# Performance work log

Measured on AMD Instinct MI355X. Metric: run time of the kernel, lower is better.

The kernel has to match this reference:

```python
import jax, jax.numpy as jnp
import numpy as np
import math

B, S, D = 4, 2048, 1024
H = 1
HD = D // H  # head_dim == hidden_dim since num_heads=1 (required by source's phase_encoder Linear)
HALF = HD // 2
SYNC_LOSS_WEIGHT = 0.01


def setup_inputs() -> dict:
    key = jax.random.key(0)
    ks = jax.random.split(key, 11)
    wstd = 0.02
    inp = {
        "x": jax.random.normal(ks[0], (B, S, D), dtype=jnp.float32),
        "Wq": jax.random.normal(ks[1], (D, D), dtype=jnp.float32) * wstd,
        "bq": jnp.zeros((D,), jnp.float32),
        "Wk": jax.random.normal(ks[2], (D, D), dtype=jnp.float32) * wstd,
        "bk": jnp.zeros((D,), jnp.float32),
        "Wv": jax.random.normal(ks[3], (D, D), dtype=jnp.float32) * wstd,
        "bv": jnp.zeros((D,), jnp.float32),
        "Wp": jax.random.normal(ks[4], (D, D), dtype=jnp.float32) * wstd,
        "bp": jnp.zeros((D,), jnp.float32),
        "Wo": jax.random.normal(ks[5], (D, D), dtype=jnp.float32) * wstd,
        "bo": jnp.zeros((D,), jnp.float32),
        "bifurcation_param": jnp.asarray(1.0, jnp.float32),
        "phase_coupling": jnp.asarray(0.5, jnp.float32),
    }
    return inp


def _phase(t, Wp, bp):
    # t: [B,H,S,HD] -> instantaneous phase via angle(complex(first_half, second_half))
    pf = t @ Wp.T + bp
    re, im = pf[..., :HALF], pf[..., HALF:]
    return jnp.arctan2(im, re)  # [B,H,S,HALF]


def reference(x, Wq, bq, Wk, bk, Wv, bv, Wp, bp, Wo, bo, bifurcation_param, phase_coupling):
    b, s, d = x.shape
    Q = (x @ Wq.T + bq).reshape(b, s, H, HD).transpose(0, 2, 1, 3)  # [B,H,S,HD]
    K = (x @ Wk.T + bk).reshape(b, s, H, HD).transpose(0, 2, 1, 3)
    V = (x @ Wv.T + bv).reshape(b, s, H, HD).transpose(0, 2, 1, 3)

    scores = jnp.einsum("bhqd,bhkd->bhqk", Q, K) / math.sqrt(HD)

    pQ = _phase(Q, Wp, bp)
    pK = _phase(K, Wp, bp)
    # mean_d cos(pQ - pK) == (cos(pQ)@cos(pK)^T + sin(pQ)@sin(pK)^T) / HALF
    sync = (jnp.einsum("bhqd,bhkd->bhqk", jnp.cos(pQ), jnp.cos(pK))
            + jnp.einsum("bhqd,bhkd->bhqk", jnp.sin(pQ), jnp.sin(pK))) / HALF

    t = jnp.tanh(scores)
    bif = bifurcation_param * t * (1.0 - t)

    chaotic = scores + phase_coupling * sync + bif
    attn = jax.nn.softmax(chaotic, axis=-1)

    av = jnp.einsum("bhqk,bhkd->bhqd", attn, V)
    av = av.transpose(0, 2, 1, 3).reshape(b, s, d)
    out = av @ Wo.T + bo

    # torch.var default: unbiased (ddof=1), over last dim of sync
    sync_loss = SYNC_LOSS_WEIGHT * jnp.var(sync, axis=-1, ddof=1).mean()
    return out, sync_loss
```

## Files before the change

kernel.cpp:

```cpp
#include <hip/hip_runtime.h>
#include <hip/hip_bf16.h>
#include <math.h>

#define S_LEN 2048
#define D_MODEL 1024
#define N_BATCH 4
#define N_HALF 512

typedef unsigned short u16;
typedef __attribute__((ext_vector_type(8))) short bf16x8;
typedef __attribute__((ext_vector_type(4))) float f32x4;

__device__ inline u16 f2bf(float v) {
  __hip_bfloat16 h = __float2bfloat16(v);
  return *reinterpret_cast<u16*>(&h);
}
__device__ inline float bf2f(u16 u) {
  __hip_bfloat16 h = *reinterpret_cast<__hip_bfloat16*>(&u);
  return __bfloat162float(h);
}
__device__ inline void gl2lds16(const void* g, void* l) {
  __builtin_amdgcn_global_load_lds(
      (const __attribute__((address_space(1))) unsigned int*)g,
      (__attribute__((address_space(3))) unsigned int*)l, 16, 0, 0);
// ... 58 lines not shown
    float v = t[c][r0 + r];
    long long idx = (long long)(bx + r0 + r) * D_MODEL + by + c;
    u16 h = f2bf(v);
    hi[idx] = h;
    lo[idx] = f2bf(v - bf2f(h));
  }
}
__global__ __launch_bounds__(256)
void w2_bias(const float* __restrict__ Wo, const float* __restrict__ bv,
             float* __restrict__ w2b) {
  const int d = blockIdx.x;
  const int tid = threadIdx.x;
  float acc = 0.f;
  for (int j = tid; j < D_MODEL; j += 256)
    acc += Wo[(long long)d * D_MODEL + j] * bv[j];
#pragma unroll
  for (int m = 1; m < 64; m <<= 1) acc += __shfl_xor(acc, m);
  __shared__ float red[4];
  if ((tid & 63) == 0) red[tid >> 6] = acc;
  __syncthreads();
  if (tid == 0) w2b[d] = red[0] + red[1] + red[2] + red[3];
}


__global__ __launch_bounds__(256, 2)
void qk_fused(const u16* __restrict__ X, const u16* __restrict__ Wq,
              const u16* __restrict__ Wk,
              const float* __restrict__ bq, const float* __restrict__ bk,
              u16* __restrict__ Qo, u16* __restrict__ Ko) {
  __shared__ u16 Xs[128 * 64];
  __shared__ u16 Qs[128 * 64];
  __shared__ u16 Ks[128 * 64];
  const int tid  = threadIdx.x;
  const int wave = tid >> 6;
  const int lane = tid & 63;
  const int quad = lane >> 4;
  const int tc   = lane & 15;
  const int bm = blockIdx.y * 128;
  const int bn = blockIdx.x * 128;
  const int wm = (wave & 1) * 64;
  const int wn = (wave >> 1) * 64;

  f32x4 acc1[4][4], acc2[4][4];
#pragma unroll
  for (int i = 0; i < 4; i++)
#pragma unroll
    for (int j = 0; j < 4; j++) {
      acc1[i][j] = (f32x4){0.f, 0.f, 0.f, 0.f};
      acc2[i][j] = (f32x4){0.f, 0.f, 0.f, 0.f};
    }

  const int srow8 = lane >> 3;
  const int scol  = ((lane & 7) ^ srow8) * 8;
  const int srowb = wave * 32;
  const u16* gx = X  + (long long)(bm + srowb + srow8) * D_MODEL + scol;
  const u16* gq = Wq + (long long)(bn + srowb + srow8) * D_MODEL + scol;
  const u16* gk = Wk + (long long)(bn + srowb + srow8) * D_MODEL + scol;
  const int wb = srowb * 64;
  const long long r8 = 8LL * D_MODEL;
  const int swzA = tc & 7;

  for (int k0 = 0; k0 < D_MODEL; k0 += 64) {
#pragma unroll
    for (int c = 0; c < 4; c++) {
      gl2lds16(gx + c * r8, Xs + wb + c * 512);
      gl2lds16(gq + c * r8, Qs + wb + c * 512);
      gl2lds16(gk + c * r8, Ks + wb + c * 512);
    }
    gx += 64; gq += 64; gk += 64;
    __syncthreads();
    bf16x8 af[4][2], bq4[4][2], bk4[4][2];
#pragma unroll
    for (int i = 0; i < 4; i++) {
      const int ra = (wm + i * 16 + tc) * 64;
      const int rb = (wn + i * 16 + tc) * 64;
#pragma unroll
      for (int ks = 0; ks < 2; ks++) {
        const int co = ((ks * 4 + quad) ^ swzA) * 8;
        af[i][ks]  = *(const bf16x8*)(Xs + ra + co);
        bq4[i][ks] = *(const bf16x8*)(Qs + rb + co);
        bk4[i][ks] = *(const bf16x8*)(Ks + rb + co);
      }
    }
#pragma unroll
    for (int i = 0; i < 4; i++)
#pragma unroll
      for (int j = 0; j < 4; j++) {
        acc1[i][j] = __builtin_amdgcn_mfma_f32_16x16x32_bf16(af[i][0], bq4[j][0], acc1[i][j], 0, 0, 0);
        acc2[i][j] = __builtin_amdgcn_mfma_f32_16x16x32_bf16(af[i][0], bk4[j][0], acc2[i][j], 0, 0, 0);
        acc1[i][j] = __builtin_amdgcn_mfma_f32_16x16x32_bf16(af[i][1], bq4[j][1], acc1[i][j], 0, 0, 0);
        acc2[i][j] = __builtin_amdgcn_mfma_f32_16x16x32_bf16(af[i][1], bk4[j][1], acc2[i][j], 0, 0, 0);
      }
    __syncthreads();
  }

#pragma unroll
  for (int i = 0; i < 4; i++) {
    const int row0 = bm + wm + i * 16 + quad * 4;
#pragma unroll
    for (int j = 0; j < 4; j++) {
      const int col = bn + wn + j * 16 + tc;
#pragma unroll
      for (int r = 0; r < 4; r++) {
        long long idx = (long long)(row0 + r) * D_MODEL + col;
        Qo[idx] = f2bf(acc1[i][j][r] + bq[col]);
        Ko[idx] = f2bf(acc2[i][j][r] + bk[col]);
      }
    }
  }
}

__global__ __launch_bounds__(256, 2)
void pf_fused(const u16* __restrict__ Qb, const u16* __restrict__ Wp,
              const float* __restrict__ bp,
              u16* __restrict__ pfQ, u16* __restrict__ pfK,
              long long TDo) {
  __shared__ u16 lds_all[3 * 128 * 64];
  u16* Qs = lds_all;
  u16* Ks = lds_all + 128 * 64;
  u16* Ws = lds_all + 2 * 128 * 64;
  const int tid  = threadIdx.x;
  const int wave = tid >> 6;
  const int lane = tid & 63;
  const int quad = lane >> 4;
  const int tc   = lane & 15;
  const int bm = blockIdx.y * 128;
  const int bn = blockIdx.x * 64;
  const int wm = (wave & 1) * 64;
  const int grp = wave >> 1;
// ... 75 lines not shown
#pragma unroll
      for (int i = 2 * half; i < 2 * half + 2; i++)
#pragma unroll
        for (int j = 0; j < 4; j++) {
          f32x4 own = *(const f32x4*)(ex + wave * 2048 + cnt * 256 + lane * 4);
          f32x4 oth = *(const f32x4*)(ex + (wave ^ 2) * 2048 + cnt * 256 + lane * 4);
          const int row0 = bm + wm + i * 16 + quad * 4;
          const long long col = colbase + j * 16 + tc;
#pragma unroll
          for (int r = 0; r < 4; r++) {
            float a = own[r], p = oth[r];
            float n2 = a * a + p * p;
            float outv = (grp == 0) ? 1.f : 0.f;
            if (n2 > 0.f) outv = a * (1.0f / sqrtf(n2));
            Ou[(long long)(row0 + r) * D_MODEL + col] = f2bf(outv);
          }
          cnt++;
        }
      __syncthreads();
    }
  }
}

__global__ __launch_bounds__(256)
void mfma_gemm_out3(const u16* __restrict__ Ah, const u16* __restrict__ Al,
                    const u16* __restrict__ Bh, const u16* __restrict__ Bl,
                    const float* __restrict__ bias, float* __restrict__ C,
                    int N, int K) {
  __shared__ u16 Ash[128 * 64];
  __shared__ u16 Asl[128 * 64];
  __shared__ u16 Bsh[128 * 64];
  __shared__ u16 Bsl[128 * 64];
  const int tid  = threadIdx.x;
  const int wave = tid >> 6;
  const int lane = tid & 63;
  const int quad = lane >> 4;
  const int tc   = lane & 15;
  const int bm = blockIdx.y * 128;
  const int bn = blockIdx.x * 128;
  const int wm = (wave & 1) * 64;
  const int wn = (wave >> 1) * 64;

  f32x4 acc[4][4];
#pragma unroll
  for (int i = 0; i < 4; i++)
#pragma unroll
    for (int j = 0; j < 4; j++) acc[i][j] = (f32x4){0.f, 0.f, 0.f, 0.f};

  const int srow8 = lane >> 3;
  const int scol  = ((lane & 7) ^ srow8) * 8;
  const int srowb = wave * 32;
  long long aoff = (long long)(bm + srowb + srow8) * K + scol;
  long long boff = (long long)(bn + srowb + srow8) * K + scol;
  const u16 *gah = Ah + aoff, *gal = Al + aoff;
  const u16 *gbh = Bh + boff, *gbl = Bl + boff;
  const int wb = srowb * 64;
  const long long r8K = 8LL * K;
  const int swzA = tc & 7;

  for (int k0 = 0; k0 < K; k0 += 64) {
#pragma unroll
    for (int c = 0; c < 4; c++) {
      gl2lds16(gah + c * r8K, Ash + wb + c * 512);
      gl2lds16(gal + c * r8K, Asl + wb + c * 512);
      gl2lds16(gbh + c * r8K, Bsh + wb + c * 512);
      gl2lds16(gbl + c * r8K, Bsl + wb + c * 512);
    }
    gah += 64; gal += 64; gbh += 64; gbl += 64;
    __syncthreads();
    bf16x8 ah[4][2], al[4][2], bh[4][2], bl[4][2];
#pragma unroll
    for (int i = 0; i < 4; i++) {
      const int ra = (wm + i * 16 + tc) * 64;
      const int rb = (wn + i * 16 + tc) * 64;
#pragma unroll
      for (int ks = 0; ks < 2; ks++) {
        const int co = ((ks * 4 + quad) ^ swzA) * 8;
        ah[i][ks] = *(const bf16x8*)(Ash + ra + co);
        al[i][ks] = *(const bf16x8*)(Asl + ra + co);
        bh[i][ks] = *(const bf16x8*)(Bsh + rb + co);
        bl[i][ks] = *(const bf16x8*)(Bsl + rb + co);
      }
    }
#pragma unroll
    for (int i = 0; i < 4; i++)
#pragma unroll
      for (int j = 0; j < 4; j++) {
#pragma unroll
        for (int ks = 0; ks < 2; ks++) {
          acc[i][j] = __builtin_amdgcn_mfma_f32_16x16x32_bf16(ah[i][ks], bh[j][ks], acc[i][j], 0, 0, 0);
          acc[i][j] = __builtin_amdgcn_mfma_f32_16x16x32_bf16(ah[i][ks], bl[j][ks], acc[i][j], 0, 0, 0);
          acc[i][j] = __builtin_amdgcn_mfma_f32_16x16x32_bf16(al[i][ks], bh[j][ks], acc[i][j], 0, 0, 0);
        }
      }
    __syncthreads();
  }
#pragma unroll
  for (int i = 0; i < 4; i++) {
    const int row0 = bm + wm + i * 16 + quad * 4;
#pragma unroll
    for (int j = 0; j < 4; j++) {
      const int col = bn + wn + j * 16 + tc;
      float b = bias ? bias[col] : 0.f;
#pragma unroll
      for (int r = 0; r < 4; r++)
        C[(long long)(row0 + r) * N + col] = acc[i][j][r] + b;
    }
  }
}

__global__ __launch_bounds__(256)
void vwt_kernel(const u16* __restrict__ W2h, const u16* __restrict__ W2l,
                const u16* __restrict__ X, const float* __restrict__ w2b,
                u16* __restrict__ Ch, u16* __restrict__ Cl,
                long long sB, long long sC) {
  __shared__ u16 Ah[128 * 64];
  __shared__ u16 Al[128 * 64];
  __shared__ u16 Bs[128 * 64];
  const int tid  = threadIdx.x;
  const int wave = tid >> 6;
  const int lane = tid & 63;
  const int quad = lane >> 4;
  const int tc   = lane & 15;
  const int bm = blockIdx.y * 128;
  const int bn = blockIdx.x * 128;
  const long long z = blockIdx.z;
  const int wm = (wave & 1) * 64;
  const int wn = (wave >> 1) * 64;

  f32x4 acc[4][4];
#pragma unroll
  for (int i = 0; i < 4; i++)
#pragma unroll
    for (int j = 0; j < 4; j++) acc[i][j] = (f32x4){0.f, 0.f, 0.f, 0.f};

  const int srow8 = lane >> 3;
  const int scol  = ((lane & 7) ^ srow8) * 8;
  const int srowb = wave * 32;
  const long long aoff = (long long)(bm + srowb + srow8) * D_MODEL + scol;
  const u16* gah = W2h + aoff;
  const u16* gal = W2l + aoff;
  const u16* gb  = X + z * sB + (long long)(bn + srowb + srow8) * D_MODEL + scol;
  const int wb = srowb * 64;
  const long long r8 = 8LL * D_MODEL;
  const int swzA = tc & 7;

  for (int k0 = 0; k0 < D_MODEL; k0 += 64) {
#pragma unroll
    for (int c = 0; c < 4; c++) {
      gl2lds16(gah + c * r8, Ah + wb + c * 512);
      gl2lds16(gal + c * r8, Al + wb + c * 512);
      gl2lds16(gb  + c * r8, Bs + wb + c * 512);
    }
    gah += 64; gal += 64; gb += 64;
    __syncthreads();
    bf16x8 ah4[4][2], al4[4][2], bx[4][2];
#pragma unroll
    for (int i = 0; i < 4; i++) {
      const int ra = (wm + i * 16 + tc) * 64;
      const int rb = (wn + i * 16 + tc) * 64;
#pragma unroll
      for (int ks = 0; ks < 2; ks++) {
        const int co = ((ks * 4 + quad) ^ swzA) * 8;
        ah4[i][ks] = *(const bf16x8*)(Ah + ra + co);
        al4[i][ks] = *(const bf16x8*)(Al + ra + co);
        bx[i][ks]  = *(const bf16x8*)(Bs + rb + co);
      }
    }
#pragma unroll
    for (int i = 0; i < 4; i++)
#pragma unroll
      for (int j = 0; j < 4; j++) {
        acc[i][j] = __builtin_amdgcn_mfma_f32_16x16x32_bf16(ah4[i][0], bx[j][0], acc[i][j], 0, 0, 0);
        acc[i][j] = __builtin_amdgcn_mfma_f32_16x16x32_bf16(al4[i][0], bx[j][0], acc[i][j], 0, 0, 0);
        acc[i][j] = __builtin_amdgcn_mfma_f32_16x16x32_bf16(ah4[i][1], bx[j][1], acc[i][j], 0, 0, 0);
        acc[i][j] = __builtin_amdgcn_mfma_f32_16x16x32_bf16(al4[i][1], bx[j][1], acc[i][j], 0, 0, 0);
      }
    __syncthreads();
  }

  u16* Chz = Ch + z * sC;
  u16* Clz = Cl + z * sC;
#pragma unroll
  for (int i = 0; i < 4; i++) {
    const int row0 = bm + wm + i * 16 + quad * 4;
#pragma unroll
    for (int j = 0; j < 4; j++) {
      const int col = bn + wn + j * 16 + tc;
#pragma unroll
      for (int r = 0; r < 4; r++) {
        float v = acc[i][j][r] + w2b[row0 + r];
        long long idx = (long long)(row0 + r) * S_LEN + col;
        u16 h = f2bf(v);
        Chz[idx] = h;
        Clz[idx] = f2bf(v - bf2f(h));
      }
    }
  }
}

__global__ __launch_bounds__(256)
void gemm_bsplit(const u16* __restrict__ A,
                 const u16* __restrict__ Bh, const u16* __restrict__ Bl,
                 const float* __restrict__ bias, float* __restrict__ C,
                 int N, int K, long long sA, long long sB, long long sC) {
  __shared__ u16 As[128 * 64];
  __shared__ u16 Bsh[128 * 64];
  __shared__ u16 Bsl[128 * 64];
  const int tid  = threadIdx.x;
  const int wave = tid >> 6;
  const int lane = tid & 63;
  const int quad = lane >> 4;
  const int tc   = lane & 15;
  const int bm = blockIdx.y * 128;
  const int bn = blockIdx.x * 128;
  const long long z = blockIdx.z;
  const int wm = (wave & 1) * 64;
  const int wn = (wave >> 1) * 64;
// ... 40 lines not shown
#pragma unroll
    for (int i = 0; i < 4; i++)
#pragma unroll
      for (int j = 0; j < 4; j++) {
        acc[i][j] = __builtin_amdgcn_mfma_f32_16x16x32_bf16(af[i][0], bh[j][0], acc[i][j], 0, 0, 0);
        acc[i][j] = __builtin_amdgcn_mfma_f32_16x16x32_bf16(af[i][0], bl[j][0], acc[i][j], 0, 0, 0);
        acc[i][j] = __builtin_amdgcn_mfma_f32_16x16x32_bf16(af[i][1], bh[j][1], acc[i][j], 0, 0, 0);
        acc[i][j] = __builtin_amdgcn_mfma_f32_16x16x32_bf16(af[i][1], bl[j][1], acc[i][j], 0, 0, 0);
      }
    __syncthreads();
  }

  float* Cz = C + z * sC;
#pragma unroll
  for (int i = 0; i < 4; i++) {
    const int row0 = bm + wm + i * 16 + quad * 4;
#pragma unroll
    for (int j = 0; j < 4; j++) {
      const int col = bn + wn + j * 16 + tc;
#pragma unroll
      for (int r = 0; r < 4; r++)
        Cz[(long long)(row0 + r) * N + col] = acc[i][j][r] + bias[col];
    }
  }
}

__global__ __launch_bounds__(256, 2)
void chaotic_fused(const u16* __restrict__ Q, const u16* __restrict__ Kt,
                   const u16* __restrict__ Uq, const u16* __restrict__ Uk,
                   float* __restrict__ Cc,
                   float* __restrict__ ssum, float* __restrict__ ssq,
                   const float* __restrict__ bifp, const float* __restrict__ pcp) {
  __shared__ u16 Qs[128 * 64];
  __shared__ u16 Ks[128 * 64];
  __shared__ u16 Us[128 * 64];
  __shared__ u16 Ws[128 * 64];
  const int tid  = threadIdx.x;
  const int wave = tid >> 6;
  const int lane = tid & 63;
  const int quad = lane >> 4;
  const int tc   = lane & 15;
  const int bm = blockIdx.y * 128;
  const int bn = blockIdx.x * 128;
  const long long z = blockIdx.z;
  const long long sQ = (long long)S_LEN * D_MODEL;
  const int wm = (wave & 1) * 64;
  const int wn = (wave >> 1) * 64;

  f32x4 acc1[4][4], acc2[4][4];
#pragma unroll
  for (int i = 0; i < 4; i++)
#pragma unroll
    for (int j = 0; j < 4; j++) {
      acc1[i][j] = (f32x4){0.f, 0.f, 0.f, 0.f};
      acc2[i][j] = (f32x4){0.f, 0.f, 0.f, 0.f};
    }

  const int srow8  = lane >> 3;
  const int scol   = ((lane & 7) ^ srow8) * 8;
  const int srowb  = wave * 32;
  const u16* gq = Q  + z * sQ + (long long)(bm + srowb + srow8) * D_MODEL + scol;
  const u16* gk = Kt + z * sQ + (long long)(bn + srowb + srow8) * D_MODEL + scol;
  const u16* gu = Uq + z * sQ + (long long)(bm + srowb + srow8) * D_MODEL + scol;
  const u16* gw = Uk + z * sQ + (long long)(bn + srowb + srow8) * D_MODEL + scol;
  const int wb = srowb * 64;
  const long long r8 = 8LL * D_MODEL;

  const int swzA = tc & 7;

  for (int k0 = 0; k0 < D_MODEL; k0 += 64) {
#pragma unroll
    for (int c = 0; c < 4; c++) {
      gl2lds16(gq + c * r8, Qs + wb + c * 512);
      gl2lds16(gk + c * r8, Ks + wb + c * 512);
      gl2lds16(gu + c * r8, Us + wb + c * 512);
      gl2lds16(gw + c * r8, Ws + wb + c * 512);
    }
    gq += 64; gk += 64; gu += 64; gw += 64;
    __syncthreads();
    {
      bf16x8 af[4][2], bg[4][2];
#pragma unroll
      for (int i = 0; i < 4; i++) {
        const int ra = (wm + i * 16 + tc) * 64;
        const int rb = (wn + i * 16 + tc) * 64;
#pragma unroll
        for (int ks = 0; ks < 2; ks++) {
          const int co = ((ks * 4 + quad) ^ swzA) * 8;
          af[i][ks] = *(const bf16x8*)(Qs + ra + co);
          bg[i][ks] = *(const bf16x8*)(Ks + rb + co);
        }
      }
#pragma unroll
      for (int i = 0; i < 4; i++)
#pragma unroll
        for (int j = 0; j < 4; j++) {
          acc1[i][j] = __builtin_amdgcn_mfma_f32_16x16x32_bf16(af[i][0], bg[j][0], acc1[i][j], 0, 0, 0);
          acc1[i][j] = __builtin_amdgcn_mfma_f32_16x16x32_bf16(af[i][1], bg[j][1], acc1[i][j], 0, 0, 0);
        }
    }
    {
      bf16x8 cf[4][2], dg[4][2];
#pragma unroll
      for (int i = 0; i < 4; i++) {
        const int ra = (wm + i * 16 + tc) * 64;
        const int rb = (wn + i * 16 + tc) * 64;
#pragma unroll
        for (int ks = 0; ks < 2; ks++) {
          const int co = ((ks * 4 + quad) ^ swzA) * 8;
          cf[i][ks] = *(const bf16x8*)(Us + ra + co);
          dg[i][ks] = *(const bf16x8*)(Ws + rb + co);
        }
      }
#pragma unroll
      for (int i = 0; i < 4; i++)
#pragma unroll
        for (int j = 0; j < 4; j++) {
          acc2[i][j] = __builtin_amdgcn_mfma_f32_16x16x32_bf16(cf[i][0], dg[j][0], acc2[i][j], 0, 0, 0);
          acc2[i][j] = __builtin_amdgcn_mfma_f32_16x16x32_bf16(cf[i][1], dg[j][1], acc2[i][j], 0, 0, 0);
        }
    }
    __syncthreads();
  }

  const float bif = *bifp;
  const float pc  = *pcp;
  float rsum[4][4], rsq[4][4];
#pragma unroll
  for (int i = 0; i < 4; i++)
#pragma unroll
    for (int r = 0; r < 4; r++) { rsum[i][r] = 0.f; rsq[i][r] = 0.f; }

  float* C = Cc + z * (long long)S_LEN * S_LEN;
#pragma unroll
  for (int i = 0; i < 4; i++) {
    const int row0 = bm + wm + i * 16 + quad * 4;
#pragma unroll
    for (int j = 0; j < 4; j++) {
      const int col = bn + wn + j * 16 + tc;
#pragma unroll
      for (int r = 0; r < 4; r++) {
        float sc = acc1[i][j][r] * 0.03125f;
        float sy = acc2[i][j][r] * (1.0f / 512.0f);
        float t  = fast_tanh(sc);
        C[(long long)(row0 + r) * S_LEN + col] = sc + pc * sy + bif * t * (1.0f - t);
        rsum[i][r] += sy;
        rsq[i][r]  += sy * sy;
      }
    }
  }
#pragma unroll
  for (int m = 1; m < 16; m <<= 1) {
#pragma unroll
    for (int i = 0; i < 4; i++)
#pragma unroll
      for (int r = 0; r < 4; r++) {
        rsum[i][r] += __shfl_xor(rsum[i][r], m);
        rsq[i][r]  += __shfl_xor(rsq[i][r], m);
      }
  }
  if (tc == 0) {
#pragma unroll
    for (int i = 0; i < 4; i++)
#pragma unroll
      for (int r = 0; r < 4; r++) {
        long long rr = z * S_LEN + bm + wm + i * 16 + quad * 4 + r;
        atomicAdd(&ssum[rr], rsum[i][r]);
        atomicAdd(&ssq[rr],  rsq[i][r]);
      }
  }
}

__global__ __launch_bounds__(256)
void softmax_bf(const float* __restrict__ Cc, u16* __restrict__ P) {
  const long long row = (long long)blockIdx.y * S_LEN + blockIdx.x;
  const int tid = threadIdx.x;
  const float* p = Cc + row * S_LEN + tid * 8;
  u16* q = P + row * S_LEN + tid * 8;
  float4 a = *(const float4*)p;
  float4 b = *(const float4*)(p + 4);
  float v[8] = {a.x, a.y, a.z, a.w, b.x, b.y, b.z, b.w};
  float m = v[0];
#pragma unroll
  for (int i = 1; i < 8; i++) m = fmaxf(m, v[i]);
#pragma unroll
  for (int mask = 1; mask < 64; mask <<= 1) m = fmaxf(m, __shfl_xor(m, mask));
  __shared__ float red[8];
  if ((tid & 63) == 0) red[tid >> 6] = m;
  __syncthreads();
  m = fmaxf(fmaxf(red[0], red[1]), fmaxf(red[2], red[3]));
  float s = 0.f;
#pragma unroll
// ... 60 lines not shown

  u16* xbf   = (u16*)d_ws;
  u16* wqb   = xbf + TD;
  u16* wkb   = wqb + WSZ;
  u16* wpb   = wkb + WSZ;
  u16* woh   = wpb + WSZ;
  u16* wol   = woh + WSZ;
  u16* wvth  = wol + WSZ;
  u16* wvtl  = wvth + WSZ;
  u16* w2h   = wvtl + WSZ;
  u16* w2l   = w2h + WSZ;
  float* W2f = (float*)(w2l + WSZ);
  float* w2b = W2f + WSZ;
  u16* Qbf   = (u16*)(w2b + D_MODEL);
  u16* Kbf   = Qbf + TD;
  u16* pfQ   = Kbf + TD;
  u16* pfK   = pfQ + TD;
  float* Cc  = (float*)(pfK + TD);
  float* ssum = Cc + (long long)N_BATCH * S_LEN * S_LEN;
  float* ssq  = ssum + NROW;
  u16* attn = Qbf;
  u16* vwh  = pfQ;
  u16* vwl  = pfK;

  dim3 blk(256);
  const long long sQ = (long long)S_LEN * D_MODEL;
  const long long sS = (long long)S_LEN * S_LEN;

  cast_bf4_multi<<<11264, blk, 0, stream>>>(x, xbf, Wq, wqb, Wk, wkb, Wp, wpb);
  cast_split<<<(int)(WSZ / 4 / 256), blk, 0, stream>>>(Wo, woh, wol, WSZ / 4);
  transpose_split<<<dim3(32, 32), blk, 0, stream>>>(Wv, wvth, wvtl);
  mfma_gemm_out3<<<dim3(8, 8, 1), blk, 0, stream>>>(
      woh, wol, wvth, wvtl, nullptr, W2f, D_MODEL, D_MODEL);
  cast_split<<<(int)(WSZ / 4 / 256), blk, 0, stream>>>(W2f, w2h, w2l, WSZ / 4);
  w2_bias<<<D_MODEL, blk, 0, stream>>>(Wo, bv, w2b);

  qk_fused<<<dim3(8, 64), blk, 0, stream>>>(xbf, wqb, wkb, bq, bk, Qbf, Kbf);
  pf_fused<<<dim3(8, 64), blk, 0, stream>>>(Qbf, wpb, bp, pfQ, pfK, TD);
  hipMemsetAsync(ssum, 0, (size_t)(2 * NROW) * sizeof(float), stream);

  chaotic_fused<<<dim3(16, 16, N_BATCH), blk, 0, stream>>>(
      Qbf, Kbf, pfQ, pfK, Cc, ssum, ssq, bifp, pcp);
  vwt_kernel<<<dim3(16, 8, N_BATCH), blk, 0, stream>>>(
      w2h, w2l, xbf, w2b, vwh, vwl, sQ, sQ);
  softmax_bf<<<dim3(S_LEN, N_BATCH), blk, 0, stream>>>(Cc, attn);
  gemm_bsplit<<<dim3(8, 16, N_BATCH), blk, 0, stream>>>(
      attn, vwh, vwl, bo, out,
      D_MODEL, S_LEN, sS, sQ, sQ);
  syncloss_kernel<<<1, 1024, 0, stream>>>(ssum, ssq, out + TD);
}
```

Before: 484.1 us.

## Merge independent GEMM launches into combined heterogeneous-block kernels

Merges the W2 = Wo·Wv split-precision GEMM into the QK projection kernel as extra blocks, and merges the chaotic score kernel with the V·W2 transform kernel into one launch with interleaved block roles. The aim is to fill the GPU better with independent work in the same launch and to cut launch gaps. The V·W2 output goes to a separate workspace buffer when space allows, because the original location aliases pfQ/pfK, which the chaotic blocks read concurrently. Otherwise it falls back to two sequential launches. The cost is more LDS per block in the merged kernels, plus possible imbalance between block types.

```diff
diff --git a/kernel.cpp b/kernel.cpp
--- a/kernel.cpp
+++ b/kernel.cpp
@@ -104,89 +104,164 @@
   if (tid == 0) w2b[d] = red[0] + red[1] + red[2] + red[3];
 }
 
-
 __global__ __launch_bounds__(256, 2)
-void qk_fused(const u16* __restrict__ X, const u16* __restrict__ Wq,
-              const u16* __restrict__ Wk,
-              const float* __restrict__ bq, const float* __restrict__ bk,
-              u16* __restrict__ Qo, u16* __restrict__ Ko) {
-  __shared__ u16 Xs[128 * 64];
-  __shared__ u16 Qs[128 * 64];
-  __shared__ u16 Ks[128 * 64];
+void qk_out3(const u16* __restrict__ X, const u16* __restrict__ Wq,
+             const u16* __restrict__ Wk,
+             const float* __restrict__ bq, const float* __restrict__ bk,
+             u16* __restrict__ Qo, u16* __restrict__ Ko,
+             const u16* __restrict__ Ah3, const u16* __restrict__ Al3,
+             const u16* __restrict__ Bh3, const u16* __restrict__ Bl3,
+             float* __restrict__ W2f) {
+  __shared__ __align__(16) u16 smem[4 * 128 * 64];
+  const int id   = blockIdx.x;
   const int tid  = threadIdx.x;
   const int wave = tid >> 6;
   const int lane = tid & 63;
   const int quad = lane >> 4;
   const int tc   = lane & 15;
-  const int bm = blockIdx.y * 128;
-  const int bn = blockIdx.x * 128;
   const int wm = (wave & 1) * 64;
   const int wn = (wave >> 1) * 64;
-
-  f32x4 acc1[4][4], acc2[4][4];
-#pragma unroll
-  for (int i = 0; i < 4; i++)
-#pragma unroll
-    for (int j = 0; j < 4; j++) {
-      acc1[i][j] = (f32x4){0.f, 0.f, 0.f, 0.f};
-      acc2[i][j] = (f32x4){0.f, 0.f, 0.f, 0.f};
-    }
-
   const int srow8 = lane >> 3;
   const int scol  = ((lane & 7) ^ srow8) * 8;
   const int srowb = wave * 32;
-  const u16* gx = X  + (long long)(bm + srowb + srow8) * D_MODEL + scol;
-  const u16* gq = Wq + (long long)(bn + srowb + srow8) * D_MODEL + scol;
-  const u16* gk = Wk + (long long)(bn + srowb + srow8) * D_MODEL + scol;
   const int wb = srowb * 64;
   const long long r8 = 8LL * D_MODEL;
   const int swzA = tc & 7;
 
-  for (int k0 = 0; k0 < D_MODEL; k0 += 64) {
-#pragma unroll
-    for (int c = 0; c < 4; c++) {
-      gl2lds16(gx + c * r8, Xs + wb + c * 512);
-      gl2lds16(gq + c * r8, Qs + wb + c * 512);
-      gl2lds16(gk + c * r8, Ks + wb + c * 512);
-    }
-    gx += 64; gq += 64; gk += 64;
-    __syncthreads();
-    bf16x8 af[4][2], bq4[4][2], bk4[4][2];
+  if (id < 64) {
+    u16* Ash = smem;
+    u16* Asl = smem + 8192;
+    u16* Bsh = smem + 16384;
+    u16* Bsl = smem + 24576;
+    const int bm = (id >> 3) * 128;
+    const int bn = (id & 7) * 128;
+
+    f32x4 acc[4][4];
+#pragma unroll
+    for (int i = 0; i < 4; i++)
+#pragma unroll
+      for (int j = 0; j < 4; j++) acc[i][j] = (f32x4){0.f, 0.f, 0.f, 0.f};
+
+    long long aoff = (long long)(bm + srowb + srow8) * D_MODEL + scol;
+    long long boff = (long long)(bn + srowb + srow8) * D_MODEL + scol;
+    const u16 *gah = Ah3 + aoff, *gal = Al3 + aoff;
+    const u16 *gbh = Bh3 + boff, *gbl = Bl3 + boff;
+
+    for (int k0 = 0; k0 < D_MODEL; k0 += 64) {
+#pragma unroll
+      for (int c = 0; c < 4; c++) {
+        gl2lds16(gah + c * r8, Ash + wb + c * 512);
+        gl2lds16(gal + c * r8, Asl + wb + c * 512);
+        gl2lds16(gbh + c * r8, Bsh + wb + c * 512);
+        gl2lds16(gbl + c * r8, Bsl + wb + c * 512);
+      }
+      gah += 64; gal += 64; gbh += 64; gbl += 64;
+      __syncthreads();
+      bf16x8 ah[4][2], al[4][2], bh[4][2], bl[4][2];
+#pragma unroll
+      for (int i = 0; i < 4; i++) {
+        const int ra = (wm + i * 16 + tc) * 64;
+        const int rb = (wn + i * 16 + tc) * 64;
+#pragma unroll
+        for (int ks = 0; ks < 2; ks++) {
+          const int co = ((ks * 4 + quad) ^ swzA) * 8;
+          ah[i][ks] = *(const bf16x8*)(Ash + ra + co);
+          al[i][ks] = *(const bf16x8*)(Asl + ra + co);
+          bh[i][ks] = *(const bf16x8*)(Bsh + rb + co);
+          bl[i][ks] = *(const bf16x8*)(Bsl + rb + co);
+        }
+      }
+#pragma unroll
+      for (int i = 0; i < 4; i++)
+#pragma unroll
+        for (int j = 0; j < 4; j++) {
+#pragma unroll
+          for (int ks = 0; ks < 2; ks++) {
+            acc[i][j] = __builtin_amdgcn_mfma_f32_16x16x32_bf16(ah[i][ks], bh[j][ks], acc[i][j], 0, 0, 0);
+            acc[i][j] = __builtin_amdgcn_mfma_f32_16x16x32_bf16(ah[i][ks], bl[j][ks], acc[i][j], 0, 0, 0);
+            acc[i][j] = __builtin_amdgcn_mfma_f32_16x16x32_bf16(al[i][ks], bh[j][ks], acc[i][j], 0, 0, 0);
+          }
+        }
+      __syncthreads();
+    }
 #pragma unroll
     for (int i = 0; i < 4; i++) {
-      const int ra = (wm + i * 16 + tc) * 64;
-      const int rb = (wn + i * 16 + tc) * 64;
-#pragma unroll
-      for (int ks = 0; ks < 2; ks++) {
-        const int co = ((ks * 4 + quad) ^ swzA) * 8;
-        af[i][ks]  = *(const bf16x8*)(Xs + ra + co);
-        bq4[i][ks] = *(const bf16x8*)(Qs + rb + co);
-        bk4[i][ks] = *(const bf16x8*)(Ks + rb + co);
-      }
-    }
+      const int row0 = bm + wm + i * 16 + quad * 4;
+#pragma unroll
+      for (int j = 0; j < 4; j++) {
+        const int col = bn + wn + j * 16 + tc;
+#pragma unroll
+        for (int r = 0; r < 4; r++)
+          W2f[(long long)(row0 + r) * D_MODEL + col] = acc[i][j][r];
+      }
+    }
+  } else {
+    u16* Xs = smem;
+    u16* Qs = smem + 8192;
+    u16* Ks = smem + 16384;
+    const int qid = id - 64;
+    const int bn = (qid & 7) * 128;
+    const int bm = (qid >> 3) * 128;
+
+    f32x4 acc1[4][4], acc2[4][4];
 #pragma unroll
     for (int i = 0; i < 4; i++)
 #pragma unroll
       for (int j = 0; j < 4; j++) {
-        acc1[i][j] = __builtin_amdgcn_mfma_f32_16x16x32_bf16(af[i][0], bq4[j][0], acc1[i][j], 0, 0, 0);
-        acc2[i][j] = __builtin_amdgcn_mfma_f32_16x16x32_bf16(af[i][0], bk4[j][0], acc2[i][j], 0, 0, 0);
-        acc1[i][j] = __builtin_amdgcn_mfma_f32_16x16x32_bf16(af[i][1], bq4[j][1], acc1[i][j], 0, 0, 0);
-        acc2[i][j] = __builtin_amdgcn_mfma_f32_16x16x32_bf16(af[i][1], bk4[j][1], acc2[i][j], 0, 0, 0);
-      }
-    __syncthreads();
-  }
-
-#pragma unroll
-  for (int i = 0; i < 4; i++) {
-    const int row0 = bm + wm + i * 16 + quad * 4;
-#pragma unroll
-    for (int j = 0; j < 4; j++) {
-      const int col = bn + wn + j * 16 + tc;
-#pragma unroll
-      for (int r = 0; r < 4; r++) {
-        long long idx = (long long)(row0 + r) * D_MODEL + col;
-        Qo[idx] = f2bf(acc1[i][j][r] + bq[col]);
-        Ko[idx] = f2bf(acc2[i][j][r] + bk[col]);
+        acc1[i][j] = (f32x4){0.f, 0.f, 0.f, 0.f};
+        acc2[i][j] = (f32x4){0.f, 0.f, 0.f, 0.f};
+      }
+
+    const u16* gx = X  + (long long)(bm + srowb + srow8) * D_MODEL + scol;
+    const u16* gq = Wq + (long long)(bn + srowb + srow8) * D_MODEL + scol;
+    const u16* gk = Wk + (long long)(bn + srowb + srow8) * D_MODEL + scol;
+
+    for (int k0 = 0; k0 < D_MODEL; k0 += 64) {
+#pragma unroll
+      for (int c = 0; c < 4; c++) {
+        gl2lds16(gx + c * r8, Xs + wb + c * 512);
+        gl2lds16(gq + c * r8, Qs + wb + c * 512);
+        gl2lds16(gk + c * r8, Ks + wb + c * 512);
+      }
+      gx += 64; gq += 64; gk += 64;
+      __syncthreads();
+      bf16x8 af[4][2], bq4[4][2], bk4[4][2];
+#pragma unroll
+      for (int i = 0; i < 4; i++) {
+        const int ra = (wm + i * 16 + tc) * 64;
+        const int rb = (wn + i * 16 + tc) * 64;
+#pragma unroll
+        for (int ks = 0; ks < 2; ks++) {
+          const int co = ((ks * 4 + quad) ^ swzA) * 8;
+          af[i][ks]  = *(const bf16x8*)(Xs + ra + co);
+          bq4[i][ks] = *(const bf16x8*)(Qs + rb + co);
+          bk4[i][ks] = *(const bf16x8*)(Ks + rb + co);
+        }
+      }
+#pragma unroll
+      for (int i = 0; i < 4; i++)
+#pragma unroll
+        for (int j = 0; j < 4; j++) {
+          acc1[i][j] = __builtin_amdgcn_mfma_f32_16x16x32_bf16(af[i][0], bq4[j][0], acc1[i][j], 0, 0, 0);
+          acc2[i][j] = __builtin_amdgcn_mfma_f32_16x16x32_bf16(af[i][0], bk4[j][0], acc2[i][j], 0, 0, 0);
+          acc1[i][j] = __builtin_amdgcn_mfma_f32_16x16x32_bf16(af[i][1], bq4[j][1], acc1[i][j], 0, 0, 0);
+          acc2[i][j] = __builtin_amdgcn_mfma_f32_16x16x32_bf16(af[i][1], bk4[j][1], acc2[i][j], 0, 0, 0);
+        }
+      __syncthreads();
+    }
+
+#pragma unroll
+    for (int i = 0; i < 4; i++) {
+      const int row0 = bm + wm + i * 16 + quad * 4;
+#pragma unroll
+      for (int j = 0; j < 4; j++) {
+        const int col = bn + wn + j * 16 + tc;
+#pragma unroll
+        for (int r = 0; r < 4; r++) {
+          long long idx = (long long)(row0 + r) * D_MODEL + col;
+          Qo[idx] = f2bf(acc1[i][j][r] + bq[col]);
+          Ko[idx] = f2bf(acc2[i][j][r] + bk[col]);
+        }
       }
     }
   }
@@ -308,178 +383,235 @@
   }
 }
 
-__global__ __launch_bounds__(256)
-void mfma_gemm_out3(const u16* __restrict__ Ah, const u16* __restrict__ Al,
-                    const u16* __restrict__ Bh, const u16* __restrict__ Bl,
-                    const float* __restrict__ bias, float* __restrict__ C,
-                    int N, int K) {
-  __shared__ u16 Ash[128 * 64];
-  __shared__ u16 Asl[128 * 64];
-  __shared__ u16 Bsh[128 * 64];
-  __shared__ u16 Bsl[128 * 64];
+__global__ __launch_bounds__(256, 2)
+void chaotic_vwt(const u16* __restrict__ Q, const u16* __restrict__ Kt,
+                 const u16* __restrict__ Uq, const u16* __restrict__ Uk,
+                 float* __restrict__ Cc,
+                 float* __restrict__ ssum, float* __restrict__ ssq,
+                 const float* __restrict__ bifp, const float* __restrict__ pcp,
+                 const u16* __restrict__ W2h, const u16* __restrict__ W2l,
+                 const u16* __restrict__ X, const float* __restrict__ w2b,
+                 u16* __restrict__ Ch, u16* __restrict__ Cl,
+                 long long sB, long long sC,
+                 int interleave, int nchao) {
+  __shared__ __align__(16) u16 smem[4 * 128 * 64];
+  const int id = blockIdx.x;
+  int cid = -1, vid = -1;
+  if (interleave) {
+    if ((id % 3) == 2) vid = id / 3;
+    else cid = (id / 3) * 2 + (id % 3);
+  } else {
+    if (id < nchao) cid = id; else vid = id - nchao;
+  }
+
   const int tid  = threadIdx.x;
   const int wave = tid >> 6;
   const int lane = tid & 63;
   const int quad = lane >> 4;
   const int tc   = lane & 15;
-  const int bm = blockIdx.y * 128;
-  const int bn = blockIdx.x * 128;
   const int wm = (wave & 1) * 64;
   const int wn = (wave >> 1) * 64;
-
-  f32x4 acc[4][4];
-#pragma unroll
-  for (int i = 0; i < 4; i++)
-#pragma unroll
-    for (int j = 0; j < 4; j++) acc[i][j] = (f32x4){0.f, 0.f, 0.f, 0.f};
-
   const int srow8 = lane >> 3;
   const int scol  = ((lane & 7) ^ srow8) * 8;
   const int srowb = wave * 32;
-  long long aoff = (long long)(bm + srowb + srow8) * K + scol;
-  long long boff = (long long)(bn + srowb + srow8) * K + scol;
-  const u16 *gah = Ah + aoff, *gal = Al + aoff;
-  const u16 *gbh = Bh + boff, *gbl = Bl + boff;
-  const int wb = srowb * 64;
-  const long long r8K = 8LL * K;
-  const int swzA = tc & 7;
-
-  for (int k0 = 0; k0 < K; k0 += 64) {
-#pragma unroll
-    for (int c = 0; c < 4; c++) {
-      gl2lds16(gah + c * r8K, Ash + wb + c * 512);
-      gl2lds16(gal + c * r8K, Asl + wb + c * 512);
-      gl2lds16(gbh + c * r8K, Bsh + wb + c * 512);
-      gl2lds16(gbl + c * r8K, Bsl + wb + c * 512);
-    }
-    gah += 64; gal += 64; gbh += 64; gbl += 64;
-    __syncthreads();
-    bf16x8 ah[4][2], al[4][2], bh[4][2], bl[4][2];
-#pragma unroll
-    for (int i = 0; i < 4; i++) {
-      const int ra = (wm + i * 16 + tc) * 64;
-      const int rb = (wn + i * 16 + tc) * 64;
-#pragma unroll
-      for (int ks = 0; ks < 2; ks++) {
-        const int co = ((ks * 4 + quad) ^ swzA) * 8;
-        ah[i][ks] = *(const bf16x8*)(Ash + ra + co);
-        al[i][ks] = *(const bf16x8*)(Asl + ra + co);
-        bh[i][ks] = *(const bf16x8*)(Bsh + rb + co);
-        bl[i][ks] = *(const bf16x8*)(Bsl + rb + co);
-      }
-    }
-#pragma unroll
-    for (int i = 0; i < 4; i++)
-#pragma unroll
-      for (int j = 0; j < 4; j++) {
-#pragma unroll
-        for (int ks = 0; ks < 2; ks++) {
-          acc[i][j] = __builtin_amdgcn_mfma_f32_16x16x32_bf16(ah[i][ks], bh[j][ks], acc[i][j], 0, 0, 0);
-          acc[i][j] = __builtin_amdgcn_mfma_f32_16x16x32_bf16(ah[i][ks], bl[j][ks], acc[i][j], 0, 0, 0);
-          acc[i][j] = __builtin_amdgcn_mfma_f32_16x16x32_bf16(al[i][ks], bh[j][ks], acc[i][j], 0, 0, 0);
-        }
-      }
-    __syncthreads();
-  }
-#pragma unroll
-  for (int i = 0; i < 4; i++) {
-    const int row0 = bm + wm + i * 16 + quad * 4;
-#pragma unroll
-    for (int j = 0; j < 4; j++) {
-      const int col = bn + wn + j * 16 + tc;
-      float b = bias ? bias[col] : 0.f;
-#pragma unroll
-      for (int r = 0; r < 4; r++)
-        C[(long long)(row0 + r) * N + col] = acc[i][j][r] + b;
-    }
-  }
-}
-
-__global__ __launch_bounds__(256)
-void vwt_kernel(const u16* __restrict__ W2h, const u16* __restrict__ W2l,
-                const u16* __restrict__ X, const float* __restrict__ w2b,
-                u16* __restrict__ Ch, u16* __restrict__ Cl,
-                long long sB, long long sC) {
-  __shared__ u16 Ah[128 * 64];
-  __shared__ u16 Al[128 * 64];
-  __shared__ u16 Bs[128 * 64];
-  const int tid  = threadIdx.x;
-  const int wave = tid >> 6;
-  const int lane = tid & 63;
-  const int quad = lane >> 4;
-  const int tc   = lane & 15;
-  const int bm = blockIdx.y * 128;
-  const int bn = blockIdx.x * 128;
-  const long long z = blockIdx.z;
-  const int wm = (wave & 1) * 64;
-  const int wn = (wave >> 1) * 64;
-
-  f32x4 acc[4][4];
-#pragma unroll
-  for (int i = 0; i < 4; i++)
-#pragma unroll
-    for (int j = 0; j < 4; j++) acc[i][j] = (f32x4){0.f, 0.f, 0.f, 0.f};
-
-  const int srow8 = lane >> 3;
-  const int scol  = ((lane & 7) ^ srow8) * 8;
-  const int srowb = wave * 32;
-  const long long aoff = (long long)(bm + srowb + srow8) * D_MODEL + scol;
-  const u16* gah = W2h + aoff;
-  const u16* gal = W2l + aoff;
-  const u16* gb  = X + z * sB + (long long)(bn + srowb + srow8) * D_MODEL + scol;
   const int wb = srowb * 64;
   const long long r8 = 8LL * D_MODEL;
   const int swzA = tc & 7;
 
-  for (int k0 = 0; k0 < D_MODEL; k0 += 64) {
-#pragma unroll
-    for (int c = 0; c < 4; c++) {
-      gl2lds16(gah + c * r8, Ah + wb + c * 512);
-      gl2lds16(gal + c * r8, Al + wb + c * 512);
-      gl2lds16(gb  + c * r8, Bs + wb + c * 512);
-    }
-    gah += 64; gal += 64; gb += 64;
-    __syncthreads();
-    bf16x8 ah4[4][2], al4[4][2], bx[4][2];
+  if (cid >= 0) {
+    u16* Qs = smem;
+    u16* Ks = smem + 8192;
+    u16* Us = smem + 16384;
+    u16* Ws = smem + 24576;
+    const int bn = (cid & 15) * 128;
+    const int bm = ((cid >> 4) & 15) * 128;
+    const long long z = cid >> 8;
+    const long long sQ = (long long)S_LEN * D_MODEL;
+
+    f32x4 acc1[4][4], acc2[4][4];
+#pragma unroll
+    for (int i = 0; i < 4; i++)
+#pragma unroll
+      for (int j = 0; j < 4; j++) {
+        acc1[i][j] = (f32x4){0.f, 0.f, 0.f, 0.f};
+        acc2[i][j] = (f32x4){0.f, 0.f, 0.f, 0.f};
+      }
+
+    const u16* gq = Q  + z * sQ + (long long)(bm + srowb + srow8) * D_MODEL + scol;
+    const u16* gk = Kt + z * sQ + (long long)(bn + srowb + srow8) * D_MODEL + scol;
+    const u16* gu = Uq + z * sQ + (long long)(bm + srowb + srow8) * D_MODEL + scol;
+    const u16* gw = Uk + z * sQ + (long long)(bn + srowb + srow8) * D_MODEL + scol;
+
+    for (int k0 = 0; k0 < D_MODEL; k0 += 64) {
+#pragma unroll
+      for (int c = 0; c < 4; c++) {
+        gl2lds16(gq + c * r8, Qs + wb + c * 512);
+        gl2lds16(gk + c * r8, Ks + wb + c * 512);
+        gl2lds16(gu + c * r8, Us + wb + c * 512);
+        gl2lds16(gw + c * r8, Ws + wb + c * 512);
+      }
+      gq += 64; gk += 64; gu += 64; gw += 64;
+      __syncthreads();
+      {
+        bf16x8 af[4][2], bg[4][2];
+#pragma unroll
+        for (int i = 0; i < 4; i++) {
+          const int ra = (wm + i * 16 + tc) * 64;
+          const int rb = (wn + i * 16 + tc) * 64;
+#pragma unroll
+          for (int ks = 0; ks < 2; ks++) {
+            const int co = ((ks * 4 + quad) ^ swzA) * 8;
+            af[i][ks] = *(const bf16x8*)(Qs + ra + co);
+            bg[i][ks] = *(const bf16x8*)(Ks + rb + co);
+          }
+        }
+#pragma unroll
+        for (int i = 0; i < 4; i++)
+#pragma unroll
+          for (int j = 0; j < 4; j++) {
+            acc1[i][j] = __builtin_amdgcn_mfma_f32_16x16x32_bf16(af[i][0], bg[j][0], acc1[i][j], 0, 0, 0);
+            acc1[i][j] = __builtin_amdgcn_mfma_f32_16x16x32_bf16(af[i][1], bg[j][1], acc1[i][j], 0, 0, 0);
+          }
+      }
+      {
+        bf16x8 cf[4][2], dg[4][2];
+#pragma unroll
+        for (int i = 0; i < 4; i++) {
+          const int ra = (wm + i * 16 + tc) * 64;
+          const int rb = (wn + i * 16 + tc) * 64;
+#pragma unroll
+          for (int ks = 0; ks < 2; ks++) {
+            const int co = ((ks * 4 + quad) ^ swzA) * 8;
+            cf[i][ks] = *(const bf16x8*)(Us + ra + co);
+            dg[i][ks] = *(const bf16x8*)(Ws + rb + co);
+          }
+        }
+#pragma unroll
+        for (int i = 0; i < 4; i++)
+#pragma unroll
+          for (int j = 0; j < 4; j++) {
+            acc2[i][j] = __builtin_amdgcn_mfma_f32_16x16x32_bf16(cf[i][0], dg[j][0], acc2[i][j], 0, 0, 0);
+            acc2[i][j] = __builtin_amdgcn_mfma_f32_16x16x32_bf16(cf[i][1], dg[j][1], acc2[i][j], 0, 0, 0);
+          }
+      }
+      __syncthreads();
+    }
+
+    const float bif = *bifp;
+    const float pc  = *pcp;
+    float rsum[4][4], rsq[4][4];
+#pragma unroll
+    for (int i = 0; i < 4; i++)
+#pragma unroll
+      for (int r = 0; r < 4; r++) { rsum[i][r] = 0.f; rsq[i][r] = 0.f; }
+
+    float* C = Cc + z * (long long)S_LEN * S_LEN;
 #pragma unroll
     for (int i = 0; i < 4; i++) {
-      const int ra = (wm + i * 16 + tc) * 64;
-      const int rb = (wn + i * 16 + tc) * 64;
-#pragma unroll
-      for (int ks = 0; ks < 2; ks++) {
-        const int co = ((ks * 4 + quad) ^ swzA) * 8;
-        ah4[i][ks] = *(const bf16x8*)(Ah + ra + co);
-        al4[i][ks] = *(const bf16x8*)(Al + ra + co);
-        bx[i][ks]  = *(const bf16x8*)(Bs + rb + co);
-      }
-    }
+      const int row0 = bm + wm + i * 16 + quad * 4;
+#pragma unroll
+      for (int j = 0; j < 4; j++) {
+        const int col = bn + wn + j * 16 + tc;
+#pragma unroll
+        for (int r = 0; r < 4; r++) {
+          float sc = acc1[i][j][r] * 0.03125f;
+          float sy = acc2[i][j][r] * (1.0f / 512.0f);
+          float t  = fast_tanh(sc);
+          C[(long long)(row0 + r) * S_LEN + col] = sc + pc * sy + bif * t * (1.0f - t);
+          rsum[i][r] += sy;
+          rsq[i][r]  += sy * sy;
+        }
+      }
+    }
+#pragma unroll
+    for (int m = 1; m < 16; m <<= 1) {
+#pragma unroll
+      for (int i = 0; i < 4; i++)
+#pragma unroll
+        for (int r = 0; r < 4; r++) {
+          rsum[i][r] += __shfl_xor(rsum[i][r], m);
+          rsq[i][r]  += __shfl_xor(rsq[i][r], m);
+        }
+    }
+    if (tc == 0) {
+#pragma unroll
+      for (int i = 0; i < 4; i++)
+#pragma unroll
+        for (int r = 0; r < 4; r++) {
+          long long rr = z * S_LEN + bm + wm + i * 16 + quad * 4 + r;
+          atomicAdd(&ssum[rr], rsum[i][r]);
+          atomicAdd(&ssq[rr],  rsq[i][r]);
+        }
+    }
+  } else {
+    u16* Ah = smem;
+    u16* Al = smem + 8192;
+    u16* Bs = smem + 16384;
+    const int bn = (vid & 15) * 128;
+    const int bm = ((vid >> 4) & 7) * 128;
+    const long long z = vid >> 7;
+
+    f32x4 acc[4][4];
 #pragma unroll
     for (int i = 0; i < 4; i++)
 #pragma unroll
+      for (int j = 0; j < 4; j++) acc[i][j] = (f32x4){0.f, 0.f, 0.f, 0.f};
+
+    const long long aoff = (long long)(bm + srowb + srow8) * D_MODEL + scol;
+    const u16* gah = W2h + aoff;
+    const u16* gal = W2l + aoff;
+    const u16* gb  = X + z * sB + (long long)(bn + srowb + srow8) * D_MODEL + scol;
+
+    for (int k0 = 0; k0 < D_MODEL; k0 += 64) {
+#pragma unroll
+      for (int c = 0; c < 4; c++) {
+        gl2lds16(gah + c * r8, Ah + wb + c * 512);
+        gl2lds16(gal + c * r8, Al + wb + c * 512);
+        gl2lds16(gb  + c * r8, Bs + wb + c * 512);
+      }
+      gah += 64; gal += 64; gb += 64;
+      __syncthreads();
+      bf16x8 ah4[4][2], al4[4][2], bx[4][2];
+#pragma unroll
+      for (int i = 0; i < 4; i++) {
+        const int ra = (wm + i * 16 + tc) * 64;
+        const int rb = (wn + i * 16 + tc) * 64;
+#pragma unroll
+        for (int ks = 0; ks < 2; ks++) {
+          const int co = ((ks * 4 + quad) ^ swzA) * 8;
+          ah4[i][ks] = *(const bf16x8*)(Ah + ra + co);
+          al4[i][ks] = *(const bf16x8*)(Al + ra + co);
+          bx[i][ks]  = *(const bf16x8*)(Bs + rb + co);
+        }
+      }
+#pragma unroll
+      for (int i = 0; i < 4; i++)
+#pragma unroll
+        for (int j = 0; j < 4; j++) {
+          acc[i][j] = __builtin_amdgcn_mfma_f32_16x16x32_bf16(ah4[i][0], bx[j][0], acc[i][j], 0, 0, 0);
+          acc[i][j] = __builtin_amdgcn_mfma_f32_16x16x32_bf16(al4[i][0], bx[j][0], acc[i][j], 0, 0, 0);
+          acc[i][j] = __builtin_amdgcn_mfma_f32_16x16x32_bf16(ah4[i][1], bx[j][1], acc[i][j], 0, 0, 0);
+          acc[i][j] = __builtin_amdgcn_mfma_f32_16x16x32_bf16(al4[i][1], bx[j][1], acc[i][j], 0, 0, 0);
+        }
+      __syncthreads();
+    }
+
+    u16* Chz = Ch + z * sC;
+    u16* Clz = Cl + z * sC;
+#pragma unroll
+    for (int i = 0; i < 4; i++) {
+      const int row0 = bm + wm + i * 16 + quad * 4;
+#pragma unroll
       for (int j = 0; j < 4; j++) {
-        acc[i][j] = __builtin_amdgcn_mfma_f32_16x16x32_bf16(ah4[i][0], bx[j][0], acc[i][j], 0, 0, 0);
-        acc[i][j] = __builtin_amdgcn_mfma_f32_16x16x32_bf16(al4[i][0], bx[j][0], acc[i][j], 0, 0, 0);
-        acc[i][j] = __builtin_amdgcn_mfma_f32_16x16x32_bf16(ah4[i][1], bx[j][1], acc[i][j], 0, 0, 0);
-        acc[i][j] = __builtin_amdgcn_mfma_f32_16x16x32_bf16(al4[i][1], bx[j][1], acc[i][j], 0, 0, 0);
-      }
-    __syncthreads();
-  }
-
-  u16* Chz = Ch + z * sC;
-  u16* Clz = Cl + z * sC;
-#pragma unroll
-  for (int i = 0; i < 4; i++) {
-    const int row0 = bm + wm + i * 16 + quad * 4;
-#pragma unroll
-    for (int j = 0; j < 4; j++) {
-      const int col = bn + wn + j * 16 + tc;
-#pragma unroll
-      for (int r = 0; r < 4; r++) {
-        float v = acc[i][j][r] + w2b[row0 + r];
-        long long idx = (long long)(row0 + r) * S_LEN + col;
-        u16 h = f2bf(v);
-        Chz[idx] = h;
-        Clz[idx] = f2bf(v - bf2f(h));
+        const int col = bn + wn + j * 16 + tc;
+#pragma unroll
+        for (int r = 0; r < 4; r++) {
+          float v = acc[i][j][r] + w2b[row0 + r];
+          long long idx = (long long)(row0 + r) * S_LEN + col;
+          u16 h = f2bf(v);
+          Chz[idx] = h;
+          Clz[idx] = f2bf(v - bf2f(h));
+        }
       }
     }
   }
@@ -566,152 +698,6 @@
       for (int r = 0; r < 4; r++)
         Cz[(long long)(row0 + r) * N + col] = acc[i][j][r] + bias[col];
     }
-  }
-}
-
-__global__ __launch_bounds__(256, 2)
-void chaotic_fused(const u16* __restrict__ Q, const u16* __restrict__ Kt,
-                   const u16* __restrict__ Uq, const u16* __restrict__ Uk,
-                   float* __restrict__ Cc,
-                   float* __restrict__ ssum, float* __restrict__ ssq,
-                   const float* __restrict__ bifp, const float* __restrict__ pcp) {
-  __shared__ u16 Qs[128 * 64];
-  __shared__ u16 Ks[128 * 64];
-  __shared__ u16 Us[128 * 64];
-  __shared__ u16 Ws[128 * 64];
-  const int tid  = threadIdx.x;
-  const int wave = tid >> 6;
-  const int lane = tid & 63;
-  const int quad = lane >> 4;
-  const int tc   = lane & 15;
-  const int bm = blockIdx.y * 128;
-  const int bn = blockIdx.x * 128;
-  const long long z = blockIdx.z;
-  const long long sQ = (long long)S_LEN * D_MODEL;
-  const int wm = (wave & 1) * 64;
-  const int wn = (wave >> 1) * 64;
-
-  f32x4 acc1[4][4], acc2[4][4];
-#pragma unroll
-  for (int i = 0; i < 4; i++)
-#pragma unroll
-    for (int j = 0; j < 4; j++) {
-      acc1[i][j] = (f32x4){0.f, 0.f, 0.f, 0.f};
-      acc2[i][j] = (f32x4){0.f, 0.f, 0.f, 0.f};
-    }
-
-  const int srow8  = lane >> 3;
-  const int scol   = ((lane & 7) ^ srow8) * 8;
-  const int srowb  = wave * 32;
-  const u16* gq = Q  + z * sQ + (long long)(bm + srowb + srow8) * D_MODEL + scol;
-  const u16* gk = Kt + z * sQ + (long long)(bn + srowb + srow8) * D_MODEL + scol;
-  const u16* gu = Uq + z * sQ + (long long)(bm + srowb + srow8) * D_MODEL + scol;
-  const u16* gw = Uk + z * sQ + (long long)(bn + srowb + srow8) * D_MODEL + scol;
-  const int wb = srowb * 64;
-  const long long r8 = 8LL * D_MODEL;
-
-  const int swzA = tc & 7;
-
-  for (int k0 = 0; k0 < D_MODEL; k0 += 64) {
-#pragma unroll
-    for (int c = 0; c < 4; c++) {
-      gl2lds16(gq + c * r8, Qs + wb + c * 512);
-      gl2lds16(gk + c * r8, Ks + wb + c * 512);
-      gl2lds16(gu + c * r8, Us + wb + c * 512);
-      gl2lds16(gw + c * r8, Ws + wb + c * 512);
-    }
-    gq += 64; gk += 64; gu += 64; gw += 64;
-    __syncthreads();
-    {
-      bf16x8 af[4][2], bg[4][2];
-#pragma unroll
-      for (int i = 0; i < 4; i++) {
-        const int ra = (wm + i * 16 + tc) * 64;
-        const int rb = (wn + i * 16 + tc) * 64;
-#pragma unroll
-        for (int ks = 0; ks < 2; ks++) {
-          const int co = ((ks * 4 + quad) ^ swzA) * 8;
-          af[i][ks] = *(const bf16x8*)(Qs + ra + co);
-          bg[i][ks] = *(const bf16x8*)(Ks + rb + co);
-        }
-      }
-#pragma unroll
-      for (int i = 0; i < 4; i++)
-#pragma unroll
-        for (int j = 0; j < 4; j++) {
-          acc1[i][j] = __builtin_amdgcn_mfma_f32_16x16x32_bf16(af[i][0], bg[j][0], acc1[i][j], 0, 0, 0);
-          acc1[i][j] = __builtin_amdgcn_mfma_f32_16x16x32_bf16(af[i][1], bg[j][1], acc1[i][j], 0, 0, 0);
-        }
-    }
-    {
-      bf16x8 cf[4][2], dg[4][2];
-#pragma unroll
-      for (int i = 0; i < 4; i++) {
-        const int ra = (wm + i * 16 + tc) * 64;
-        const int rb = (wn + i * 16 + tc) * 64;
-#pragma unroll
-        for (int ks = 0; ks < 2; ks++) {
-          const int co = ((ks * 4 + quad) ^ swzA) * 8;
-          cf[i][ks] = *(const bf16x8*)(Us + ra + co);
-          dg[i][ks] = *(const bf16x8*)(Ws + rb + co);
-        }
-      }
-#pragma unroll
-      for (int i = 0; i < 4; i++)
-#pragma unroll
-        for (int j = 0; j < 4; j++) {
-          acc2[i][j] = __builtin_amdgcn_mfma_f32_16x16x32_bf16(cf[i][0], dg[j][0], acc2[i][j], 0, 0, 0);
-          acc2[i][j] = __builtin_amdgcn_mfma_f32_16x16x32_bf16(cf[i][1], dg[j][1], acc2[i][j], 0, 0, 0);
-        }
-    }
-    __syncthreads();
-  }
-
-  const float bif = *bifp;
-  const float pc  = *pcp;
-  float rsum[4][4], rsq[4][4];
-#pragma unroll
-  for (int i = 0; i < 4; i++)
-#pragma unroll
-    for (int r = 0; r < 4; r++) { rsum[i][r] = 0.f; rsq[i][r] = 0.f; }
-
-  float* C = Cc + z * (long long)S_LEN * S_LEN;
-#pragma unroll
-  for (int i = 0; i < 4; i++) {
-    const int row0 = bm + wm + i * 16 + quad * 4;
-#pragma unroll
-    for (int j = 0; j < 4; j++) {
-      const int col = bn + wn + j * 16 + tc;
-#pragma unroll
-      for (int r = 0; r < 4; r++) {
-        float sc = acc1[i][j][r] * 0.03125f;
-        float sy = acc2[i][j][r] * (1.0f / 512.0f);
-        float t  = fast_tanh(sc);
-        C[(long long)(row0 + r) * S_LEN + col] = sc + pc * sy + bif * t * (1.0f - t);
-        rsum[i][r] += sy;
-        rsq[i][r]  += sy * sy;
-      }
-    }
-  }
-#pragma unroll
-  for (int m = 1; m < 16; m <<= 1) {
-#pragma unroll
-    for (int i = 0; i < 4; i++)
-#pragma unroll
-      for (int r = 0; r < 4; r++) {
-        rsum[i][r] += __shfl_xor(rsum[i][r], m);
-        rsq[i][r]  += __shfl_xor(rsq[i][r], m);
-      }
-  }
-  if (tc == 0) {
-#pragma unroll
-    for (int i = 0; i < 4; i++)
-#pragma unroll
-      for (int r = 0; r < 4; r++) {
-        long long rr = z * S_LEN + bm + wm + i * 16 + quad * 4 + r;
-        atomicAdd(&ssum[rr], rsum[i][r]);
-        atomicAdd(&ssq[rr],  rsq[i][r]);
-      }
   }
 }
 
@@ -818,6 +804,10 @@
   u16* attn = Qbf;
   u16* vwh  = pfQ;
   u16* vwl  = pfK;
+  u16* vwh2 = (u16*)(ssq + NROW);
+  u16* vwl2 = vwh2 + TD;
+  const size_t need = (size_t)((char*)(vwl2 + TD) - (char*)d_ws);
+  const bool fused = (ws_size >= need);
 
   dim3 blk(256);
   const long long sQ = (long long)S_LEN * D_MODEL;
@@ -826,22 +816,30 @@
   cast_bf4_multi<<<11264, blk, 0, stream>>>(x, xbf, Wq, wqb, Wk, wkb, Wp, wpb);
   cast_split<<<(int)(WSZ / 4 / 256), blk, 0, stream>>>(Wo, woh, wol, WSZ / 4);
   transpose_split<<<dim3(32, 32), blk, 0, stream>>>(Wv, wvth, wvtl);
-  mfma_gemm_out3<<<dim3(8, 8, 1), blk, 0, stream>>>(
-      woh, wol, wvth, wvtl, nullptr, W2f, D_MODEL, D_MODEL);
+  qk_out3<<<576, blk, 0, stream>>>(xbf, wqb, wkb, bq, bk, Qbf, Kbf,
+                                   woh, wol, wvth, wvtl, W2f);
   cast_split<<<(int)(WSZ / 4 / 256), blk, 0, stream>>>(W2f, w2h, w2l, WSZ / 4);
   w2_bias<<<D_MODEL, blk, 0, stream>>>(Wo, bv, w2b);
 
-  qk_fused<<<dim3(8, 64), blk, 0, stream>>>(xbf, wqb, wkb, bq, bk, Qbf, Kbf);
   pf_fused<<<dim3(8, 64), blk, 0, stream>>>(Qbf, wpb, bp, pfQ, pfK, TD);
   hipMemsetAsync(ssum, 0, (size_t)(2 * NROW) * sizeof(float), stream);
 
-  chaotic_fused<<<dim3(16, 16, N_BATCH), blk, 0, stream>>>(
-      Qbf, Kbf, pfQ, pfK, Cc, ssum, ssq, bifp, pcp);
-  vwt_kernel<<<dim3(16, 8, N_BATCH), blk, 0, stream>>>(
-      w2h, w2l, xbf, w2b, vwh, vwl, sQ, sQ);
+  if (fused) {
+    chaotic_vwt<<<1536, blk, 0, stream>>>(
+        Qbf, Kbf, pfQ, pfK, Cc, ssum, ssq, bifp, pcp,
+        w2h, w2l, xbf, w2b, vwh2, vwl2, sQ, sQ, 1, 1024);
+  } else {
+    chaotic_vwt<<<1024, blk, 0, stream>>>(
+        Qbf, Kbf, pfQ, pfK, Cc, ssum, ssq, bifp, pcp,
+        w2h, w2l, xbf, w2b, vwh, vwl, sQ, sQ, 0, 1024);
+    chaotic_vwt<<<512, blk, 0, stream>>>(
+        Qbf, Kbf, pfQ, pfK, Cc, ssum, ssq, bifp, pcp,
+        w2h, w2l, xbf, w2b, vwh, vwl, sQ, sQ, 0, 0);
+  }
+
   softmax_bf<<<dim3(S_LEN, N_BATCH), blk, 0, stream>>>(Cc, attn);
   gemm_bsplit<<<dim3(8, 16, N_BATCH), blk, 0, stream>>>(
-      attn, vwh, vwl, bo, out,
+      attn, fused ? vwh2 : vwh, fused ? vwl2 : vwl, bo, out,
       D_MODEL, S_LEN, sS, sQ, sQ);
   syncloss_kernel<<<1, 1024, 0, stream>>>(ssum, ssq, out + TD);
 }
```

New measurement: 472.9 us. -2.3%, faster.
